# Performance work log

Hardware: AMD Instinct MI355X
Metric: run time of the kernel (lower is better)

## Reference

```python
import math
import jax, jax.numpy as jnp
import numpy as np

TOP_K = 2
N_EXP = 8
EVAL_CAPACITY_FACTOR = 2.0
MIN_CAPACITY = 4


def setup_inputs() -> dict:
    key = jax.random.key(0)
    k1, k2 = jax.random.split(key)
    x = jax.random.normal(k1, (2, 2048, 1024), dtype=jnp.float32)
    # nn.Linear(n_embd, n_experts, bias=False) weight: [n_exp, n_embd]
    w_g = jax.random.normal(k2, (N_EXP, 1024), dtype=jnp.float32) * 0.02
    return {"x": x, "w_g": w_g}


def reference(x, w_g):
    B, T, H = x.shape
    N = B * T                      # num_tokens
    E = w_g.shape[0]               # n_experts
    K = TOP_K
    capacity = max(int(math.floor(K * EVAL_CAPACITY_FACTOR * N / E)), MIN_CAPACITY)

    x_flat = x.reshape(N, H)
    logits = x_flat @ w_g.T                      # [N, E]

    top_k_logits, top_k_idx = jax.lax.top_k(logits, K)   # [N, K]

    # scatter top-k logits into a -inf canvas, then softmax over experts
    router_probs = jnp.full_like(logits, -jnp.inf)
    router_probs = router_probs.at[jnp.arange(N)[:, None], top_k_idx].set(top_k_logits)
    router_probs = jax.nn.softmax(router_probs, axis=-1)  # [N, E]

    # capacity-based dispatch
    exp_mask = jax.nn.one_hot(top_k_idx, E, dtype=jnp.int32)   # [N, K, E]
    exp_mask = jnp.transpose(exp_mask, (1, 0, 2))              # [K, N, E]

    exp_rank = jnp.cumsum(exp_mask.reshape(K * N, E), axis=0) - 1
    exp_rank = exp_rank.reshape(K, N, E)                       # position within expert

    exp_mask = exp_mask * (exp_rank < capacity).astype(jnp.int32)
    used_capacity = jnp.sum(exp_mask, axis=(0, 1))             # [E]

    exp_rank_tok = jnp.sum(exp_mask * exp_rank, axis=-1)       # [K, N]

    exp_weights = exp_mask.astype(router_probs.dtype) * router_probs[None]  # [K, N, E]
    exp_rank_sc = jax.nn.one_hot(exp_rank_tok, capacity, dtype=router_probs.dtype)  # [K, N, C]

    cb_weight = jnp.einsum('kne,knc->nec', exp_weights, exp_rank_sc)  # [N, E, C]
    sec_mask = cb_weight.astype(bool)
    return used_capacity, cb_weight, sec_mask
```

## Files before the change

### kernel.cpp

```cpp
#include <hip/hip_runtime.h>
#include <math.h>


#define HDIM 1024
#define NEXP 8

__global__ __launch_bounds__(256) void logits_topk_kernel(
    const float* __restrict__ x, const float* __restrict__ wg,
    int* __restrict__ expert_slot, float* __restrict__ prob_slot, int N) {
  __shared__ float w_lds[NEXP * HDIM];
  const int tid = threadIdx.x;
  for (int i = tid; i < NEXP * HDIM; i += blockDim.x) w_lds[i] = wg[i];
  __syncthreads();

  const int wave = tid >> 6;
  const int lane = tid & 63;
  const int n = blockIdx.x * 4 + wave;
  if (n >= N) return;

  const float* xr = x + (size_t)n * HDIM;
  float acc[NEXP];
#pragma unroll
  for (int e = 0; e < NEXP; e++) acc[e] = 0.0f;

  for (int j = 0; j < HDIM; j += 64) {
    float xv = xr[j + lane];
#pragma unroll
    for (int e = 0; e < NEXP; e++) acc[e] += xv * w_lds[e * HDIM + j + lane];
  }

#pragma unroll
  for (int e = 0; e < NEXP; e++) {
    float v = acc[e];
    for (int off = 32; off > 0; off >>= 1) v += __shfl_down(v, off, 64);
    acc[e] = v;
  }

  if (lane == 0) {
    int b0 = 0;
    float v0 = acc[0];
#pragma unroll
    for (int e = 1; e < NEXP; e++) {
      if (acc[e] > v0) { v0 = acc[e]; b0 = e; }
    }
    int b1 = -1;
    float v1 = -INFINITY;
#pragma unroll
    for (int e = 0; e < NEXP; e++) {
      if (e == b0) continue;
      if (acc[e] > v1) { v1 = acc[e]; b1 = e; }
    }
    float e2 = expf(v1 - v0);
    float p0 = 1.0f / (1.0f + e2);
    float p1 = e2 / (1.0f + e2);
    expert_slot[n] = b0;
    expert_slot[N + n] = b1;
    prob_slot[n] = p0;
    prob_slot[N + n] = p1;
  }
}

__global__ __launch_bounds__(512) void dispatch_kernel(
    const int* __restrict__ expert_slot, const float* __restrict__ prob_slot,
    float* __restrict__ used_cap, float* __restrict__ cb,
    float* __restrict__ sec, int N, int C) {
  const int w = threadIdx.x >> 6;
  const int lane = threadIdx.x & 63;
  if (w >= NEXP) return;

  const int S = 2 * N;
  const unsigned long long below_mask = (lane == 63) ? 0x7FFFFFFFFFFFFFFFull
                                                     : ((1ull << lane) - 1ull);
  int prefix = 0;
  for (int base = 0; base < S; base += 256) {
    int s0 = base + lane;
    int s1 = base + 64 + lane;
    int s2 = base + 128 + lane;
    int s3 = base + 192 + lane;
    int e0 = expert_slot[s0];
    int e1 = expert_slot[s1];
    int e2 = expert_slot[s2];
    int e3 = expert_slot[s3];
#pragma unroll
    for (int u = 0; u < 4; u++) {
      int s = (u == 0) ? s0 : (u == 1) ? s1 : (u == 2) ? s2 : s3;
      int e = (u == 0) ? e0 : (u == 1) ? e1 : (u == 2) ? e2 : e3;
      bool match = (e == w);
      unsigned long long m = __ballot(match);
      int rank = prefix + __popcll(m & below_mask);
      if (match && rank < C) {
        int n = (s >= N) ? (s - N) : s;
        size_t off = ((size_t)n * NEXP + w) * (size_t)C + (size_t)rank;
        cb[off] = prob_slot[s];
        sec[off] = 1.0f;
      }
      prefix += __popcll(m);
    }
  }
  if (lane == 0) used_cap[w] = (float)(prefix < C ? prefix : C);
}

extern "C" void kernel_launch(void* const* d_in, const int* in_sizes, int n_in,
                              void* d_out, int out_size, void* d_ws, size_t ws_size,
                              hipStream_t stream) {
  const float* x = (const float*)d_in[0];
  const float* wg = (const float*)d_in[1];

  const int N = in_sizes[0] / HDIM;
  const int K = 2;
  int capacity = (int)floor((double)K * 2.0 * (double)N / (double)NEXP);
  if (capacity < 4) capacity = 4;

  float* out = (float*)d_out;
  float* used_cap = out;
  float* cb = out + NEXP;
  float* sec = cb + (size_t)N * NEXP * (size_t)capacity;

  int* expert_slot = (int*)d_ws;
  float* prob_slot = (float*)((char*)d_ws + sizeof(int) * (size_t)(2 * N));

  hipMemsetAsync(d_out, 0, sizeof(float) * (size_t)out_size, stream);

  logits_topk_kernel<<<(N + 3) / 4, 256, 0, stream>>>(x, wg, expert_slot,
                                                      prob_slot, N);
  dispatch_kernel<<<1, 512, 0, stream>>>(expert_slot, prob_slot, used_cap, cb,
                                         sec, N, capacity);
}
```

Measured before the change: 584.9 us.

## Replace memset plus scatter with compact rank table and dense vectorized output writer

The dispatch step now records only a per-(token, expert) rank and weight into a compact workspace table. A new elementwise kernel writes the full combine-weight and mask tensors with float4 stores in one pass. This removes the separate full-output memset and the scattered single-float stores. It adds one kernel launch and initialisation of the rank table inside the single-block kernel.

```diff
diff --git a/kernel.cpp b/kernel.cpp
--- a/kernel.cpp
+++ b/kernel.cpp
@@ -60,14 +60,16 @@
   }
 }
 
-__global__ __launch_bounds__(512) void dispatch_kernel(
+__global__ __launch_bounds__(512) void rank_kernel(
     const int* __restrict__ expert_slot, const float* __restrict__ prob_slot,
-    float* __restrict__ used_cap, float* __restrict__ cb,
-    float* __restrict__ sec, int N, int C) {
-  const int w = threadIdx.x >> 6;
-  const int lane = threadIdx.x & 63;
-  if (w >= NEXP) return;
+    float* __restrict__ used_cap, int* __restrict__ rank_t,
+    float* __restrict__ val_t, int N, int C) {
+  const int tid = threadIdx.x;
+  for (int i = tid; i < N * NEXP; i += 512) rank_t[i] = -1;
+  __syncthreads();
 
+  const int w = tid >> 6;
+  const int lane = tid & 63;
   const int S = 2 * N;
   const unsigned long long below_mask = (lane == 63) ? 0x7FFFFFFFFFFFFFFFull
                                                      : ((1ull << lane) - 1ull);
@@ -90,14 +92,32 @@
       int rank = prefix + __popcll(m & below_mask);
       if (match && rank < C) {
         int n = (s >= N) ? (s - N) : s;
-        size_t off = ((size_t)n * NEXP + w) * (size_t)C + (size_t)rank;
-        cb[off] = prob_slot[s];
-        sec[off] = 1.0f;
+        rank_t[n * NEXP + w] = rank;
+        val_t[n * NEXP + w] = prob_slot[s];
       }
       prefix += __popcll(m);
     }
   }
   if (lane == 0) used_cap[w] = (float)(prefix < C ? prefix : C);
+}
+
+__global__ __launch_bounds__(256) void write_out_kernel(
+    const int* __restrict__ rank_t, const float* __restrict__ val_t,
+    float* __restrict__ cb, float* __restrict__ sec, int C4, int total4) {
+  int t = blockIdx.x * 256 + threadIdx.x;
+  if (t >= total4) return;
+  int row = t / C4;
+  int c4 = t - row * C4;
+  int rk = rank_t[row];
+  float4 v = {0.0f, 0.0f, 0.0f, 0.0f};
+  float4 s = {0.0f, 0.0f, 0.0f, 0.0f};
+  if ((rk >> 2) == c4) {
+    float val = val_t[row];
+    ((float*)&v)[rk & 3] = val;
+    ((float*)&s)[rk & 3] = (val != 0.0f) ? 1.0f : 0.0f;
+  }
+  ((float4*)cb)[t] = v;
+  ((float4*)sec)[t] = s;
 }
 
 extern "C" void kernel_launch(void* const* d_in, const int* in_sizes, int n_in,
@@ -116,13 +136,18 @@
   float* cb = out + NEXP;
   float* sec = cb + (size_t)N * NEXP * (size_t)capacity;
 
-  int* expert_slot = (int*)d_ws;
-  float* prob_slot = (float*)((char*)d_ws + sizeof(int) * (size_t)(2 * N));
-
-  hipMemsetAsync(d_out, 0, sizeof(float) * (size_t)out_size, stream);
+  char* ws = (char*)d_ws;
+  int* expert_slot = (int*)ws;
+  float* prob_slot = (float*)(ws + 4 * (size_t)(2 * N));
+  int* rank_t = (int*)(ws + 8 * (size_t)(2 * N));
+  float* val_t = (float*)(ws + 8 * (size_t)(2 * N) + 4 * (size_t)(N * NEXP));
 
   logits_topk_kernel<<<(N + 3) / 4, 256, 0, stream>>>(x, wg, expert_slot,
                                                       prob_slot, N);
-  dispatch_kernel<<<1, 512, 0, stream>>>(expert_slot, prob_slot, used_cap, cb,
-                                         sec, N, capacity);
+  rank_kernel<<<1, 512, 0, stream>>>(expert_slot, prob_slot, used_cap, rank_t,
+                                     val_t, N, capacity);
+  int C4 = capacity / 4;
+  int total4 = N * NEXP * C4;
+  write_out_kernel<<<(total4 + 255) / 256, 256, 0, stream>>>(rank_t, val_t, cb,
+                                                             sec, C4, total4);
 }
```

Measured after the change: 614.3 us. 5.0% more time.

## Parallelize capacity dispatch into count/scan/scatter kernels and vectorize logits loads

Applied to the files above, without the earlier changes.

Replaces the single-block serial dispatch loop with three kernels: per-64-slot expert counts via ballot, a single-block prefix scan over chunk counts, and a fully parallel scatter that computes each slot's rank from its chunk base plus an in-wave ballot popcount. The logits kernel also switches to float4 loads for both the gate weights in LDS and the token rows. The aim is to remove the serialized pass over all slots that ran on one workgroup. The cost is two extra kernel launches plus small workspace traffic for counts and bases. The large output memset still runs and is unchanged.

```diff
diff --git a/kernel.cpp b/kernel.cpp
--- a/kernel.cpp
+++ b/kernel.cpp
@@ -10,7 +10,8 @@
     int* __restrict__ expert_slot, float* __restrict__ prob_slot, int N) {
   __shared__ float w_lds[NEXP * HDIM];
   const int tid = threadIdx.x;
-  for (int i = tid; i < NEXP * HDIM; i += blockDim.x) w_lds[i] = wg[i];
+  for (int i = tid; i < NEXP * HDIM / 4; i += blockDim.x)
+    ((float4*)w_lds)[i] = ((const float4*)wg)[i];
   __syncthreads();
 
   const int wave = tid >> 6;
@@ -23,10 +24,14 @@
 #pragma unroll
   for (int e = 0; e < NEXP; e++) acc[e] = 0.0f;
 
-  for (int j = 0; j < HDIM; j += 64) {
-    float xv = xr[j + lane];
 #pragma unroll
-    for (int e = 0; e < NEXP; e++) acc[e] += xv * w_lds[e * HDIM + j + lane];
+  for (int j = 0; j < HDIM; j += 256) {
+    float4 xv = ((const float4*)(xr + j))[lane];
+#pragma unroll
+    for (int e = 0; e < NEXP; e++) {
+      float4 wv = ((const float4*)(w_lds + e * HDIM + j))[lane];
+      acc[e] += xv.x * wv.x + xv.y * wv.y + xv.z * wv.z + xv.w * wv.w;
+    }
   }
 
 #pragma unroll
@@ -60,44 +65,72 @@
   }
 }
 
-__global__ __launch_bounds__(512) void dispatch_kernel(
-    const int* __restrict__ expert_slot, const float* __restrict__ prob_slot,
-    float* __restrict__ used_cap, float* __restrict__ cb,
-    float* __restrict__ sec, int N, int C) {
+__global__ __launch_bounds__(256) void count_kernel(
+    const int* __restrict__ expert_slot, int* __restrict__ counts, int S) {
+  const int gid = blockIdx.x * 256 + threadIdx.x;
+  const int wave = gid >> 6;
+  const int lane = gid & 63;
+  const int s = wave * 64 + lane;
+  if (s >= S) return;
+  const int e = expert_slot[s];
+#pragma unroll
+  for (int w = 0; w < NEXP; w++) {
+    unsigned long long m = __ballot(e == w);
+    if (lane == w) counts[wave * NEXP + w] = __popcll(m);
+  }
+}
+
+__global__ __launch_bounds__(512) void scan_kernel(
+    const int* __restrict__ counts, int* __restrict__ base,
+    float* __restrict__ used_cap, int nchunk, int C) {
   const int w = threadIdx.x >> 6;
   const int lane = threadIdx.x & 63;
-  if (w >= NEXP) return;
 
-  const int S = 2 * N;
-  const unsigned long long below_mask = (lane == 63) ? 0x7FFFFFFFFFFFFFFFull
-                                                     : ((1ull << lane) - 1ull);
-  int prefix = 0;
-  for (int base = 0; base < S; base += 256) {
-    int s0 = base + lane;
-    int s1 = base + 64 + lane;
-    int s2 = base + 128 + lane;
-    int s3 = base + 192 + lane;
-    int e0 = expert_slot[s0];
-    int e1 = expert_slot[s1];
-    int e2 = expert_slot[s2];
-    int e3 = expert_slot[s3];
+  int v0 = (lane < nchunk) ? counts[lane * NEXP + w] : 0;
+  int s0 = v0;
+  for (int off = 1; off < 64; off <<= 1) {
+    int t = __shfl_up(s0, off, 64);
+    if (lane >= off) s0 += t;
+  }
+  int total0 = __shfl(s0, 63, 64);
+  if (lane < nchunk) base[lane * NEXP + w] = s0 - v0;
+
+  int i1 = 64 + lane;
+  int v1 = (i1 < nchunk) ? counts[i1 * NEXP + w] : 0;
+  int s1 = v1;
+  for (int off = 1; off < 64; off <<= 1) {
+    int t = __shfl_up(s1, off, 64);
+    if (lane >= off) s1 += t;
+  }
+  if (i1 < nchunk) base[i1 * NEXP + w] = total0 + s1 - v1;
+  int total = total0 + __shfl(s1, 63, 64);
+  if (lane == 0) used_cap[w] = (float)(total < C ? total : C);
+}
+
+__global__ __launch_bounds__(256) void scatter_kernel(
+    const int* __restrict__ expert_slot, const float* __restrict__ prob_slot,
+    const int* __restrict__ base, float* __restrict__ cb,
+    float* __restrict__ sec, int N, int C) {
+  const int gid = blockIdx.x * 256 + threadIdx.x;
+  const int wave = gid >> 6;
+  const int lane = gid & 63;
+  const int s = wave * 64 + lane;
+  if (s >= 2 * N) return;
+  const int e = expert_slot[s];
+  const float p = prob_slot[s];
+  const unsigned long long below = (1ull << lane) - 1ull;
+  int rank = -1;
 #pragma unroll
-    for (int u = 0; u < 4; u++) {
-      int s = (u == 0) ? s0 : (u == 1) ? s1 : (u == 2) ? s2 : s3;
-      int e = (u == 0) ? e0 : (u == 1) ? e1 : (u == 2) ? e2 : e3;
-      bool match = (e == w);
-      unsigned long long m = __ballot(match);
-      int rank = prefix + __popcll(m & below_mask);
-      if (match && rank < C) {
-        int n = (s >= N) ? (s - N) : s;
-        size_t off = ((size_t)n * NEXP + w) * (size_t)C + (size_t)rank;
-        cb[off] = prob_slot[s];
-        sec[off] = 1.0f;
-      }
-      prefix += __popcll(m);
-    }
+  for (int w = 0; w < NEXP; w++) {
+    unsigned long long m = __ballot(e == w);
+    if (e == w) rank = base[wave * NEXP + w] + __popcll(m & below);
   }
-  if (lane == 0) used_cap[w] = (float)(prefix < C ? prefix : C);
+  if (rank < C) {
+    int n = (s >= N) ? (s - N) : s;
+    size_t off = ((size_t)n * NEXP + e) * (size_t)C + (size_t)rank;
+    cb[off] = p;
+    sec[off] = (p != 0.0f) ? 1.0f : 0.0f;
+  }
 }
 
 extern "C" void kernel_launch(void* const* d_in, const int* in_sizes, int n_in,
@@ -111,18 +144,27 @@
   int capacity = (int)floor((double)K * 2.0 * (double)N / (double)NEXP);
   if (capacity < 4) capacity = 4;
 
+  const int S = 2 * N;
+  const int nchunk = (S + 63) / 64;
+
   float* out = (float*)d_out;
   float* used_cap = out;
   float* cb = out + NEXP;
   float* sec = cb + (size_t)N * NEXP * (size_t)capacity;
 
-  int* expert_slot = (int*)d_ws;
-  float* prob_slot = (float*)((char*)d_ws + sizeof(int) * (size_t)(2 * N));
+  char* ws = (char*)d_ws;
+  int* expert_slot = (int*)ws;
+  float* prob_slot = (float*)(ws + 4 * (size_t)S);
+  int* counts = (int*)(ws + 8 * (size_t)S);
+  int* base = (int*)(ws + 8 * (size_t)S + 4 * (size_t)(nchunk * NEXP));
 
   hipMemsetAsync(d_out, 0, sizeof(float) * (size_t)out_size, stream);
 
   logits_topk_kernel<<<(N + 3) / 4, 256, 0, stream>>>(x, wg, expert_slot,
                                                       prob_slot, N);
-  dispatch_kernel<<<1, 512, 0, stream>>>(expert_slot, prob_slot, used_cap, cb,
-                                         sec, N, capacity);
+  count_kernel<<<(S + 255) / 256, 256, 0, stream>>>(expert_slot, counts, S);
+  scan_kernel<<<1, 512, 0, stream>>>(counts, base, used_cap, nchunk, capacity);
+  scatter_kernel<<<(S + 255) / 256, 256, 0, stream>>>(expert_slot, prob_slot,
+                                                      base, cb, sec, N,
+                                                      capacity);
 }
```

Result: faster. 534.6 us (-8.6%).
